# Kernel tuning notes

Hardware: AMD Instinct MI355X
Metric: run time of the kernel (lower is better)

The kernel has to match this reference:

```python
import jax, jax.numpy as jnp
import numpy as np

V, D, K, NH, FF, NV, MC, NL = 4096, 128, 3, 4, 512, 16384, 32, 2
HD = D // NH


def _ln(x, g, b):
    m = x.mean(-1, keepdims=True)
    v = ((x - m) ** 2).mean(-1, keepdims=True)
    return (x - m) / jnp.sqrt(v + 1e-5) * g + b


def setup_inputs() -> dict:
    key = jax.random.key(0)
    ks = iter(jax.random.split(key, 48))
    r = lambda shape, s=1.0: jax.random.normal(next(ks), shape, jnp.float32) * s
    inp = {}
    inp["visits"] = jax.random.randint(next(ks), (NV, MC), 0, V)
    inp["deltas"] = jax.random.uniform(next(ks), (NV,), jnp.float32) * 365.0
    inp["pad_idx"] = 0
    inp["X_hyp"] = r((V, D), 0.03)  # points inside unit Poincare ball
    inp["kernels"] = r((K, V, V), 1.0 / np.sqrt(V))
    inp["proj_W"] = r((K * D, D), 1.0 / np.sqrt(K * D))
    inp["proj_b"] = jnp.zeros((D,), jnp.float32)
    for nm in ["Wq", "Wk", "Wv", "Wo"]:
        inp[nm] = r((NL, D, D), 1.0 / np.sqrt(D))
    for nm in ["bq", "bk", "bv", "bo"]:
        inp[nm] = jnp.zeros((NL, D), jnp.float32)
    inp["ff_W1"] = r((NL, D, FF), 1.0 / np.sqrt(D))
    inp["ff_b1"] = jnp.zeros((NL, FF), jnp.float32)
    inp["ff_W2"] = r((NL, FF, D), 1.0 / np.sqrt(FF))
    inp["ff_b2"] = jnp.zeros((NL, D), jnp.float32)
    inp["ln1_g"] = jnp.ones((NL, D), jnp.float32)
    inp["ln1_b"] = jnp.zeros((NL, D), jnp.float32)
    inp["ln2_g"] = jnp.ones((NL, D), jnp.float32)
    inp["ln2_b"] = jnp.zeros((NL, D), jnp.float32)
    inp["tf_W"] = r((1, D))
    inp["tf_b"] = jnp.zeros((D,), jnp.float32)
    inp["tp_W"] = r((D, D), 1.0 / np.sqrt(D))
    inp["tp_b"] = jnp.zeros((D,), jnp.float32)
    return inp


def reference(visits, deltas, pad_idx, X_hyp, kernels, proj_W, proj_b,
              Wq, Wk, Wv, Wo, bq, bk, bv, bo,
              ff_W1, ff_b1, ff_W2, ff_b2,
              ln1_g, ln1_b, ln2_g, ln2_b,
              tf_W, tf_b, tp_W, tp_b):
    # --- hyperbolic logmap0 (Poincare ball, c=1) ---
    nrm = jnp.clip(jnp.linalg.norm(X_hyp, axis=-1, keepdims=True), 1e-7, 1.0 - 1e-5)
    Z0 = jnp.arctanh(nrm) * X_hyp / nrm  # [V, D]
    # --- multi-scale graph diffusion + projection ---
    Zk = jnp.einsum('kvu,ud->vkd', kernels, Z0).reshape(V, K * D)  # concat over scales
    H = Zk @ proj_W + proj_b  # [V, D]
    # --- global self-attention blocks over all codes (batch 1, L=V) ---
    x = H[None]  # [1, V, D]
    for i in range(NL):
        q = (x @ Wq[i] + bq[i]).reshape(1, V, NH, HD).transpose(0, 2, 1, 3)
        k = (x @ Wk[i] + bk[i]).reshape(1, V, NH, HD).transpose(0, 2, 1, 3)
        v = (x @ Wv[i] + bv[i]).reshape(1, V, NH, HD).transpose(0, 2, 1, 3)
        a = jax.nn.softmax(jnp.einsum('bhqd,bhkd->bhqk', q, k) / np.sqrt(HD), axis=-1)
        o = jnp.einsum('bhqk,bhkd->bhqd', a, v).transpose(0, 2, 1, 3).reshape(1, V, D)
        o = o @ Wo[i] + bo[i]
        x = _ln(x + o, ln1_g[i], ln1_b[i])
        f = jax.nn.gelu(x @ ff_W1[i] + ff_b1[i], approximate=False) @ ff_W2[i] + ff_b2[i]
        x = _ln(x + f, ln2_g[i], ln2_b[i])
    Hr = x[0]  # [V, D]
    # --- time embedding ---
    freq = (deltas[:, None] / 180.0) @ tf_W + tf_b  # [NV, D]
    te = (1.0 - jnp.tanh(freq) ** 2) @ tp_W + tp_b
    # --- ragged per-visit gather + masked mean (the fused-kernel target) ---
    mask = (visits != pad_idx)  # [NV, MC]
    hg = Hr[visits] * mask[..., None]  # [NV, MC, D]
    cnt = mask.sum(-1, keepdims=True)
    vis = hg.sum(1) / jnp.maximum(cnt, 1)  # empty visits -> zeros
    return vis + te
```

## Files before the change

kernel.cpp:

```cpp
#include <hip/hip_runtime.h>


using f16 = _Float16;
typedef f16   f16x8 __attribute__((ext_vector_type(8)));
typedef float f32x4 __attribute__((ext_vector_type(4)));

#define V_   4096
#define D_   128
#define NVIS 16384
#define KS_  8

union H4 { f16 h[4]; uint2 u; };

struct CvtTask { const float* src; void* dst; int R, C, kind; };
struct CvtTasks { CvtTask t[24]; int n; };

__global__ __launch_bounds__(256) void cvt_kernel(CvtTasks T) {
  int tid0 = blockIdx.x * 256 + threadIdx.x;
  int stride = gridDim.x * 256;
  for (int i = 0; i < T.n; i++) {
    CvtTask tk = T.t[i];
    int total = tk.R * tk.C;
    for (int idx = tid0; idx < total; idx += stride) {
      int r = idx / tk.C, c = idx - r * tk.C;
      if (tk.kind == 0)
        ((f16*)tk.dst)[(long long)c * tk.R + r] = (f16)tk.src[idx];
      else
        ((float*)tk.dst)[idx] = tk.src[idx];
    }
  }
}

__global__ __launch_bounds__(256) void logmap_kernel(const float* __restrict__ X, float* __restrict__ Z0) {
  int row = blockIdx.x * 4 + (threadIdx.x >> 6);
  int l = threadIdx.x & 63;
  const float* xr = X + (long long)row * D_;
  float a = xr[l], b = xr[l + 64];
  float ss = a * a + b * b;
  #pragma unroll
  for (int m = 1; m < 64; m <<= 1) ss += __shfl_xor(ss, m);
  float nrm = sqrtf(ss);
  float nc = fminf(fmaxf(nrm, 1e-7f), 1.0f - 1e-5f);
  float scale = atanhf(nc) / nc;
  float* zr = Z0 + (long long)row * D_;
  zr[l] = a * scale; zr[l + 64] = b * scale;
}

struct GemmP {
  const float* A;  long long a_y, a_z;  int lda;
  const f16*  BT;  long long bt_y, bt_z; int ldbt;
  const float* bias; int bias_y, bias_z;
  float* C;  long long c_y, c_z;   int ldc;
  f16*  CH;  long long ch_y, ch_z; int ldch;
  f16*  CHT; long long cht_y, cht_z; int ldcht;
  int K;
};

template<int ACT, bool WC, bool WH, bool WHT>
__global__ __launch_bounds__(256) void gemm_kernel(GemmP p) {
  __shared__ alignas(16) f16 As[64][64];
  __shared__ alignas(16) f16 Bs[128][64];
  int tid = threadIdx.x;
  int m0 = blockIdx.x * 64;
  long long by = blockIdx.y, bz = blockIdx.z;
  const float* A = p.A + by * p.a_y + bz * p.a_z + (long long)m0 * p.lda;
  const f16* BT  = p.BT + by * p.bt_y + bz * p.bt_z;

  int wid = tid >> 6, l = tid & 63;
  int lr = l & 15, lg = l >> 4;
  int wm = (wid & 1) * 32;
  int wn = (wid >> 1) * 64;

  f32x4 acc[2][4] = {};

  for (int kb = 0; kb < p.K; kb += 64) {
    __syncthreads();
    #pragma unroll
    for (int pi = 0; pi < 4; pi++) {
      int idx = pi * 256 + tid;
      int r = idx >> 4, c4 = (idx & 15) * 4;
      float4 v = *(const float4*)(A + (long long)r * p.lda + kb + c4);
      int cc = c4 ^ ((r & 7) << 3);
      H4 tmp; tmp.h[0] = (f16)v.x; tmp.h[1] = (f16)v.y; tmp.h[2] = (f16)v.z; tmp.h[3] = (f16)v.w;
      *(uint2*)&As[r][cc] = tmp.u;
    }
    #pragma unroll
    for (int pi = 0; pi < 4; pi++) {
      int idx = pi * 256 + tid;
      int n = idx >> 3, g8 = (idx & 7) * 8;
      f16x8 v = *(const f16x8*)(BT + (long long)n * p.ldbt + kb + g8);
      *(f16x8*)&Bs[n][g8 ^ ((n & 7) << 3)] = v;
    }
    __syncthreads();
    #pragma unroll
    for (int kk = 0; kk < 64; kk += 32) {
      f16x8 a[2], b[4];
      #pragma unroll
      for (int mt = 0; mt < 2; mt++) {
        int r = wm + mt * 16 + lr;
        a[mt] = *(const f16x8*)&As[r][(kk + lg * 8) ^ ((r & 7) << 3)];
      }
      #pragma unroll
      for (int nt = 0; nt < 4; nt++) {
        int n = wn + nt * 16 + lr;
        b[nt] = *(const f16x8*)&Bs[n][(kk + lg * 8) ^ ((n & 7) << 3)];
      }
      #pragma unroll
      for (int mt = 0; mt < 2; mt++)
        #pragma unroll
        for (int nt = 0; nt < 4; nt++)
          acc[mt][nt] = __builtin_amdgcn_mfma_f32_16x16x32_f16(a[mt], b[nt], acc[mt][nt], 0, 0, 0);
    }
  }

  const float* bias = p.bias ? p.bias + by * p.bias_y + bz * p.bias_z : nullptr;
  float* C = nullptr; f16* CH = nullptr; f16* CHT = nullptr;
  if (WC)  C   = p.C   + by * p.c_y   + bz * p.c_z   + (long long)m0 * p.ldc;
  if (WH)  CH  = p.CH  + by * p.ch_y  + bz * p.ch_z  + (long long)m0 * p.ldch;
  if (WHT) CHT = p.CHT + by * p.cht_y + bz * p.cht_z;

  #pragma unroll
  for (int nt = 0; nt < 4; nt++) {
    int n = wn + nt * 16 + lr;
    float bv = bias ? bias[n] : 0.0f;
    #pragma unroll
    for (int mt = 0; mt < 2; mt++) {
      H4 th;
      #pragma unroll
      for (int r = 0; r < 4; r++) {
        float val = acc[mt][nt][r] + bv;
        if (ACT == 1) val = 0.5f * val * (1.0f + erff(val * 0.70710678118654752f));
        int m = wm + mt * 16 + lg * 4 + r;
        if (WC) C[(long long)m * p.ldc + n] = val;
        if (WH) CH[(long long)m * p.ldch + n] = (f16)val;
        th.h[r] = (f16)val;
      }
      if (WHT)
        *(uint2*)&CHT[(long long)n * p.ldcht + m0 + wm + mt * 16 + lg * 4] = th.u;
    }
  }
}

__global__ __launch_bounds__(256) void combine_kernel(const float* __restrict__ Hp, const float* __restrict__ proj_b,
                                                      float* __restrict__ x) {
  int i = blockIdx.x * 256 + threadIdx.x;
  float s = proj_b[i & 127];
  #pragma unroll
  for (int j = 0; j < 12; j++) s += Hp[(long long)j * (V_ * D_) + i];
  x[i] = s;
}

__global__ __launch_bounds__(256) void attn_kernel(const f16* __restrict__ qh, const f16* __restrict__ kh,
                                                   const f16* __restrict__ vT,
                                                   float* __restrict__ Op, float* __restrict__ Ml) {
  __shared__ alignas(16) f16 Ks[64][40];
  __shared__ alignas(16) f16 Vs[32][72];
  __shared__ alignas(16) f16 Ps[4][16][72];
  int tid = threadIdx.x, w = tid >> 6, l = tid & 63, lr = l & 15, lg = l >> 4;
  int h = blockIdx.y, q0 = blockIdx.x * 64, z = blockIdx.z;
  const float sc = 0.17677669529663687f;

  f16x8 aq = *(const f16x8*)&qh[(long long)(q0 + w * 16 + lr) * D_ + h * 32 + lg * 8];
  float mrow[4], lsum[4];
  f32x4 oacc[2] = {};
  #pragma unroll
  for (int r = 0; r < 4; r++) { mrow[r] = -1e30f; lsum[r] = 0.f; }
  const f32x4 vzero = {0.f, 0.f, 0.f, 0.f};

  for (int kt = z * (V_ / 64 / KS_); kt < (z + 1) * (V_ / 64 / KS_); kt++) {
    int key0 = kt * 64;
    __syncthreads();
    {
      int key = tid >> 2, g8 = (tid & 3) * 8;
      *(f16x8*)&Ks[key][g8] = *(const f16x8*)&kh[(long long)(key0 + key) * D_ + h * 32 + g8];
      int dd = tid >> 3, kg = (tid & 7) * 8;
      *(f16x8*)&Vs[dd][kg] = *(const f16x8*)&vT[(long long)(h * 32 + dd) * V_ + key0 + kg];
    }
    __syncthreads();
    f32x4 s[4];
    #pragma unroll
    for (int t = 0; t < 4; t++) {
      f16x8 bk = *(const f16x8*)&Ks[t * 16 + lr][lg * 8];
      s[t] = __builtin_amdgcn_mfma_f32_16x16x32_f16(aq, bk, vzero, 0, 0, 0);
    }
    float pv[4][4];
    #pragma unroll
    for (int r = 0; r < 4; r++) {
      float sv0 = s[0][r] * sc, sv1 = s[1][r] * sc, sv2 = s[2][r] * sc, sv3 = s[3][r] * sc;
      float mx = fmaxf(fmaxf(sv0, sv1), fmaxf(sv2, sv3));
      #pragma unroll
      for (int msk = 1; msk < 16; msk <<= 1) mx = fmaxf(mx, __shfl_xor(mx, msk));
      float mn = fmaxf(mrow[r], mx);
      float alpha = expf(mrow[r] - mn);
      float e0 = expf(sv0 - mn), e1 = expf(sv1 - mn), e2 = expf(sv2 - mn), e3 = expf(sv3 - mn);
      pv[0][r] = e0; pv[1][r] = e1; pv[2][r] = e2; pv[3][r] = e3;
      float rs = e0 + e1 + e2 + e3;
      #pragma unroll
      for (int msk = 1; msk < 16; msk <<= 1) rs += __shfl_xor(rs, msk);
      lsum[r] = lsum[r] * alpha + rs;
      mrow[r] = mn;
      oacc[0][r] *= alpha; oacc[1][r] *= alpha;
    }
    #pragma unroll
    for (int t = 0; t < 4; t++)
      #pragma unroll
      for (int r = 0; r < 4; r++)
        Ps[w][lg * 4 + r][t * 16 + lr] = (f16)pv[t][r];
    #pragma unroll
    for (int kc = 0; kc < 2; kc++) {
      f16x8 pa = *(const f16x8*)&Ps[w][lr][kc * 32 + lg * 8];
      #pragma unroll
      for (int t = 0; t < 2; t++) {
        f16x8 bvv = *(const f16x8*)&Vs[t * 16 + lr][kc * 32 + lg * 8];
        oacc[t] = __builtin_amdgcn_mfma_f32_16x16x32_f16(pa, bvv, oacc[t], 0, 0, 0);
      }
    }
  }
  #pragma unroll
  for (int t = 0; t < 2; t++)
    #pragma unroll
    for (int r = 0; r < 4; r++) {
      int q = q0 + w * 16 + lg * 4 + r;
      Op[(long long)z * (V_ * D_) + (long long)q * D_ + h * 32 + t * 16 + lr] = oacc[t][r];
    }
  if (lr == 0) {
    #pragma unroll
    for (int r = 0; r < 4; r++) {
      int q = q0 + w * 16 + lg * 4 + r;
      Ml[(z * 4 + h) * V_ + q] = mrow[r];
      Ml[KS_ * 4 * V_ + (z * 4 + h) * V_ + q] = lsum[r];
    }
  }
}

__global__ __launch_bounds__(256) void attn_combine(const float* __restrict__ Op, const float* __restrict__ Ml,
                                                    float* __restrict__ o) {
  int i = blockIdx.x * 256 + threadIdx.x;
  int q = i >> 7, h = (i & 127) >> 5;
  float mv[KS_], lv[KS_];
  float m = -1e30f;
  #pragma unroll
  for (int s = 0; s < KS_; s++) {
    mv[s] = Ml[(s * 4 + h) * V_ + q];
    lv[s] = Ml[KS_ * 4 * V_ + (s * 4 + h) * V_ + q];
    m = fmaxf(m, mv[s]);
  }
  float L = 0.f, O = 0.f;
  #pragma unroll
  for (int s = 0; s < KS_; s++) {
    float wgt = expf(mv[s] - m);
    L += wgt * lv[s];
    O += wgt * Op[(long long)s * (V_ * D_) + i];
  }
  o[i] = O / L;
}

__global__ __launch_bounds__(256) void ln_kernel(float* __restrict__ x, const float* __restrict__ add,
                                                 const float* __restrict__ g, const float* __restrict__ b) {
  int row = blockIdx.x * 4 + (threadIdx.x >> 6);
  int l = threadIdx.x & 63;
  long long base = (long long)row * D_;
  float a = x[base + l] + add[base + l];
  float c = x[base + l + 64] + add[base + l + 64];
  float s = a + c, ss = a * a + c * c;
  #pragma unroll
  for (int m = 1; m < 64; m <<= 1) { s += __shfl_xor(s, m); ss += __shfl_xor(ss, m); }
  float mean = s * (1.0f / 128.0f);
  float var = ss * (1.0f / 128.0f) - mean * mean;
  float rstd = rsqrtf(var + 1e-5f);
  x[base + l]      = (a - mean) * rstd * g[l] + b[l];
  x[base + l + 64] = (c - mean) * rstd * g[l + 64] + b[l + 64];
}

__global__ __launch_bounds__(256) void timefeat_kernel(const float* __restrict__ deltas, const float* __restrict__ tf_W,
                                                       const float* __restrict__ tf_b, float* __restrict__ S) {
  int i = blockIdx.x * 256 + threadIdx.x;
  int n = i >> 7, d = i & 127;
  float fr = deltas[n] * (1.0f / 180.0f) * tf_W[d] + tf_b[d];
  float t = tanhf(fr);
  S[i] = 1.0f - t * t;
}

__global__ __launch_bounds__(256) void gather_kernel(const int* __restrict__ visits, const int* __restrict__ pad_ptr,
                                                     const float* __restrict__ Hr, float* __restrict__ out) {
  __shared__ int vis[2][32];
  int tid = threadIdx.x;
  int pad = *pad_ptr;
  int nb = blockIdx.x * 2;
  if (tid < 64) { int s = tid >> 5, c = tid & 31; vis[s][c] = visits[(long long)(nb + s) * 32 + c]; }
  __syncthreads();
  int s = tid >> 7, d = tid & 127;
  float acc = 0.f; int cnt = 0;
  #pragma unroll 8
  for (int c = 0; c < 32; c++) {
    int idx = vis[s][c];
    if (idx != pad) { acc += Hr[(long long)idx * D_ + d]; cnt++; }
  }
  long long oi = (long long)(nb + s) * D_ + d;
  out[oi] += acc / (float)(cnt > 0 ? cnt : 1);
}

extern "C" void kernel_launch(void* const* d_in, const int* in_sizes, int n_in,
                              void* d_out, int out_size, void* d_ws, size_t ws_size,
                              hipStream_t stream) {
  const int*   visits  = (const int*)d_in[0];
  const float* deltas  = (const float*)d_in[1];
  const int*   pad_idx = (const int*)d_in[2];
  const float* X_hyp   = (const float*)d_in[3];
  const float* kernels = (const float*)d_in[4];
  const float* proj_W  = (const float*)d_in[5];
  const float* proj_b  = (const float*)d_in[6];
  const float* Wq = (const float*)d_in[7];
  const float* Wk = (const float*)d_in[8];
  const float* Wv = (const float*)d_in[9];
  const float* Wo = (const float*)d_in[10];
  const float* bq = (const float*)d_in[11];
  const float* bk = (const float*)d_in[12];
  const float* bv = (const float*)d_in[13];
  const float* bo = (const float*)d_in[14];
  const float* ff_W1 = (const float*)d_in[15];
  const float* ff_b1 = (const float*)d_in[16];
  const float* ff_W2 = (const float*)d_in[17];
  const float* ff_b2 = (const float*)d_in[18];
  const float* ln1_g = (const float*)d_in[19];
  const float* ln1_b = (const float*)d_in[20];
  const float* ln2_g = (const float*)d_in[21];
  const float* ln2_b = (const float*)d_in[22];
  const float* tf_W  = (const float*)d_in[23];
  const float* tf_b  = (const float*)d_in[24];
  const float* tp_W  = (const float*)d_in[25];
  const float* tp_b  = (const float*)d_in[26];
  float* out = (float*)d_out;

  char* ws = (char*)d_ws;
  constexpr long long MB = 1ll << 20;
  f16*   projT = (f16*)(ws);
  f16*   qkvT  = (f16*)(ws + 98304);
  f16*   woT   = (f16*)(ws + 294912);
  f16*   w1T   = (f16*)(ws + 360448);
  f16*   w2T   = (f16*)(ws + 622592);
  f16*   tpT   = (f16*)(ws + 884736);
  float* bqkv  = (float*)(ws + 917504);
  float* Z0    = (float*)(ws + 1 * MB);
  f16*   ycatT = (f16*)(ws + 3 * MB);
  float* x     = (float*)(ws + 6 * MB);
  char*  big   = ws + 8 * MB;
  float* Hp    = (float*)big;
  f16*   qk_h  = (f16*)big;
  f16*   vT    = (f16*)(big + 2 * MB);
  float* o_    = (float*)(big + 3 * MB);
  float* oW    = (float*)(big + 5 * MB);
  float* Op    = (float*)(big + 7 * MB);
  float* Ml    = (float*)(big + 23 * MB);
  float* t_    = (float*)big;
  float* f_    = (float*)(big + 8 * MB);
  float* S_    = (float*)big;
  (void)ws_size; (void)in_sizes; (void)n_in; (void)out_size;

  CvtTasks T; int ntk = 0;
  auto addT = [&](const float* s, void* d, int R, int C, int kind) { T.t[ntk++] = {s, d, R, C, kind}; };
  for (int k = 0; k < 3; k++) addT(proj_W + k * 16384, projT + k * 16384, 128, 128, 0);
  for (int i = 0; i < 2; i++) {
    addT(Wq + i * 16384, qkvT + i * 49152 + 0,     128, 128, 0);
    addT(Wk + i * 16384, qkvT + i * 49152 + 16384, 128, 128, 0);
    addT(Wv + i * 16384, qkvT + i * 49152 + 32768, 128, 128, 0);
    addT(Wo + i * 16384, woT + i * 16384, 128, 128, 0);
    addT(ff_W1 + i * 65536, w1T + i * 65536, 128, 512, 0);
    addT(ff_W2 + i * 65536, w2T + i * 65536, 512, 128, 0);
    addT(bq + i * 128, bqkv + i * 384 + 0,   1, 128, 1);
    addT(bk + i * 128, bqkv + i * 384 + 128, 1, 128, 1);
    addT(bv + i * 128, bqkv + i * 384 + 256, 1, 128, 1);
  }
  addT(tp_W, tpT, 128, 128, 0);
  T.n = ntk;
  cvt_kernel<<<256, 256, 0, stream>>>(T);

  logmap_kernel<<<V_ / 4, 256, 0, stream>>>(X_hyp, Z0);

  {
    GemmP g{};
    g.A = Z0; g.lda = 128;
    g.BT = projT; g.ldbt = 128; g.bt_z = 16384;
    g.CHT = ycatT; g.ldcht = V_; g.cht_z = (long long)128 * V_;
    g.K = 128;
    gemm_kernel<0, false, false, true><<<dim3(64, 1, 3), 256, 0, stream>>>(g);
  }
  {
    GemmP g{};
    g.A = kernels; g.lda = V_; g.a_y = 1024; g.a_z = (long long)V_ * V_;
    g.BT = ycatT;  g.ldbt = V_; g.bt_y = 1024; g.bt_z = (long long)128 * V_;
    g.C = Hp; g.ldc = 128; g.c_y = (long long)V_ * D_; g.c_z = 4ll * V_ * D_;
    g.K = 1024;
    gemm_kernel<0, true, false, false><<<dim3(64, 4, 3), 256, 0, stream>>>(g);
  }
  combine_kernel<<<V_ * D_ / 256, 256, 0, stream>>>(Hp, proj_b, x);

  for (int i = 0; i < 2; i++) {
    {
      GemmP g{};
      g.A = x; g.lda = 128;
      g.BT = qkvT + i * 49152; g.ldbt = 128; g.bt_z = 16384;
      g.bias = bqkv + i * 384; g.bias_z = 128;
      g.CH = qk_h; g.ldch = 128; g.ch_z = (long long)V_ * D_;
      g.K = 128;
      gemm_kernel<0, false, true, false><<<dim3(64, 1, 2), 256, 0, stream>>>(g);
    }
    {
      GemmP g{};
      g.A = x; g.lda = 128;
      g.BT = qkvT + i * 49152 + 32768; g.ldbt = 128;
      g.bias = bqkv + i * 384 + 256;
      g.CHT = vT; g.ldcht = V_;
      g.K = 128;
      gemm_kernel<0, false, false, true><<<dim3(64, 1, 1), 256, 0, stream>>>(g);
    }
    attn_kernel<<<dim3(V_ / 64, 4, KS_), 256, 0, stream>>>(qk_h, qk_h + (long long)V_ * D_, vT, Op, Ml);
    attn_combine<<<V_ * D_ / 256, 256, 0, stream>>>(Op, Ml, o_);
    {
      GemmP g{};
      g.A = o_; g.lda = 128;
      g.BT = woT + i * 16384; g.ldbt = 128;
      g.bias = bo + i * 128;
      g.C = oW; g.ldc = 128;
      g.K = 128;
      gemm_kernel<0, true, false, false><<<dim3(64, 1, 1), 256, 0, stream>>>(g);
    }
    ln_kernel<<<V_ / 4, 256, 0, stream>>>(x, oW, ln1_g + i * 128, ln1_b + i * 128);
    {
      GemmP g{};
      g.A = x; g.lda = 128;
      g.BT = w1T + i * 65536; g.ldbt = 128; g.bt_y = 128 * 128;
      g.bias = ff_b1 + i * 512; g.bias_y = 128;
      g.C = t_; g.ldc = 512; g.c_y = 128;
      g.K = 128;
      gemm_kernel<1, true, false, false><<<dim3(64, 4, 1), 256, 0, stream>>>(g);
    }
    {
      GemmP g{};
      g.A = t_; g.lda = 512;
      g.BT = w2T + i * 65536; g.ldbt = 512;
      g.bias = ff_b2 + i * 128;
      g.C = f_; g.ldc = 128;
      g.K = 512;
      gemm_kernel<0, true, false, false><<<dim3(64, 1, 1), 256, 0, stream>>>(g);
    }
    ln_kernel<<<V_ / 4, 256, 0, stream>>>(x, f_, ln2_g + i * 128, ln2_b + i * 128);
  }

  timefeat_kernel<<<NVIS * D_ / 256, 256, 0, stream>>>(deltas, tf_W, tf_b, S_);
  {
    GemmP g{};
    g.A = S_; g.lda = 128;
    g.BT = tpT; g.ldbt = 128;
    g.bias = tp_b;
    g.C = out; g.ldc = 128;
    g.K = 128;
    gemm_kernel<0, true, false, false><<<dim3(NVIS / 64, 1, 1), 256, 0, stream>>>(g);
  }
  gather_kernel<<<NVIS / 2, 256, 0, stream>>>(visits, pad_idx, x, out);
}
```

Baseline: 708.9 us.

## Fuse residual+LayerNorm into GEMM epilogue, merge QKV GEMMs, transpose attention softmax

Moves the residual add and LayerNorm into the Wo and FF2 GEMM epilogues, reducing row statistics across warps through shared memory, and removes the separate ln_kernel launches and intermediate buffers. Merges the QK and V projection GEMMs into one launch with per-z output modes. Computes attention scores transposed so each lane owns one query row, cutting the per-row shuffle reductions and allowing vectorized P stores. This adds a __syncthreads and extra shared memory to the GEMM epilogue.

Result: faster. 640.0 us (-9.7%).

```diff
diff --git a/kernel.cpp b/kernel.cpp
--- a/kernel.cpp
+++ b/kernel.cpp
@@ -53,13 +53,15 @@
   float* C;  long long c_y, c_z;   int ldc;
   f16*  CH;  long long ch_y, ch_z; int ldch;
   f16*  CHT; long long cht_y, cht_z; int ldcht;
+  const float* lng; const float* lnb;
   int K;
 };
 
-template<int ACT, bool WC, bool WH, bool WHT>
+template<int EPI>
 __global__ __launch_bounds__(256) void gemm_kernel(GemmP p) {
   __shared__ alignas(16) f16 As[64][64];
   __shared__ alignas(16) f16 Bs[128][64];
+  __shared__ float lnred[2][64][2];
   int tid = threadIdx.x;
   int m0 = blockIdx.x * 64;
   long long by = blockIdx.y, bz = blockIdx.z;
@@ -114,29 +116,80 @@
   }
 
   const float* bias = p.bias ? p.bias + by * p.bias_y + bz * p.bias_z : nullptr;
-  float* C = nullptr; f16* CH = nullptr; f16* CHT = nullptr;
-  if (WC)  C   = p.C   + by * p.c_y   + bz * p.c_z   + (long long)m0 * p.ldc;
-  if (WH)  CH  = p.CH  + by * p.ch_y  + bz * p.ch_z  + (long long)m0 * p.ldch;
-  if (WHT) CHT = p.CHT + by * p.cht_y + bz * p.cht_z;
-
-  #pragma unroll
-  for (int nt = 0; nt < 4; nt++) {
-    int n = wn + nt * 16 + lr;
-    float bv = bias ? bias[n] : 0.0f;
-    #pragma unroll
-    for (int mt = 0; mt < 2; mt++) {
-      H4 th;
+
+  if constexpr (EPI == 5) {
+    float* C = p.C + (long long)m0 * p.ldc;
+    #pragma unroll
+    for (int nt = 0; nt < 4; nt++) {
+      int n = wn + nt * 16 + lr;
+      float bv = bias ? bias[n] : 0.0f;
+      #pragma unroll
+      for (int mt = 0; mt < 2; mt++)
+        #pragma unroll
+        for (int r = 0; r < 4; r++) {
+          int m = wm + mt * 16 + lg * 4 + r;
+          acc[mt][nt][r] += bv + C[(long long)m * p.ldc + n];
+        }
+    }
+    #pragma unroll
+    for (int mt = 0; mt < 2; mt++)
       #pragma unroll
       for (int r = 0; r < 4; r++) {
-        float val = acc[mt][nt][r] + bv;
-        if (ACT == 1) val = 0.5f * val * (1.0f + erff(val * 0.70710678118654752f));
-        int m = wm + mt * 16 + lg * 4 + r;
-        if (WC) C[(long long)m * p.ldc + n] = val;
-        if (WH) CH[(long long)m * p.ldch + n] = (f16)val;
-        th.h[r] = (f16)val;
-      }
-      if (WHT)
-        *(uint2*)&CHT[(long long)n * p.ldcht + m0 + wm + mt * 16 + lg * 4] = th.u;
+        float s = 0.f, ss = 0.f;
+        #pragma unroll
+        for (int nt = 0; nt < 4; nt++) { float v = acc[mt][nt][r]; s += v; ss += v * v; }
+        #pragma unroll
+        for (int msk = 1; msk < 16; msk <<= 1) { s += __shfl_xor(s, msk); ss += __shfl_xor(ss, msk); }
+        if (lr == 0) {
+          int row = wm + mt * 16 + lg * 4 + r;
+          lnred[wid >> 1][row][0] = s; lnred[wid >> 1][row][1] = ss;
+        }
+      }
+    __syncthreads();
+    #pragma unroll
+    for (int mt = 0; mt < 2; mt++)
+      #pragma unroll
+      for (int r = 0; r < 4; r++) {
+        int row = wm + mt * 16 + lg * 4 + r;
+        float s  = lnred[0][row][0] + lnred[1][row][0];
+        float ss = lnred[0][row][1] + lnred[1][row][1];
+        float mean = s * (1.0f / 128.0f);
+        float rstd = rsqrtf(ss * (1.0f / 128.0f) - mean * mean + 1e-5f);
+        #pragma unroll
+        for (int nt = 0; nt < 4; nt++) {
+          int n = wn + nt * 16 + lr;
+          C[(long long)row * p.ldc + n] = (acc[mt][nt][r] - mean) * rstd * p.lng[n] + p.lnb[n];
+        }
+      }
+    return;
+  } else {
+    bool do_c  = (EPI == 0 || EPI == 1);
+    bool do_h  = (EPI == 4 && bz < 2);
+    bool do_ht = (EPI == 3) || (EPI == 4 && bz == 2);
+    float* C = nullptr; f16* CH = nullptr; f16* CHT = nullptr;
+    if (do_c)  C   = p.C   + by * p.c_y   + bz * p.c_z   + (long long)m0 * p.ldc;
+    if (do_h)  CH  = p.CH  + by * p.ch_y  + bz * p.ch_z  + (long long)m0 * p.ldch;
+    if (do_ht) CHT = p.CHT + by * p.cht_y + bz * p.cht_z;
+
+    #pragma unroll
+    for (int nt = 0; nt < 4; nt++) {
+      int n = wn + nt * 16 + lr;
+      float bv = bias ? bias[n] : 0.0f;
+      #pragma unroll
+      for (int mt = 0; mt < 2; mt++) {
+        H4 th;
+        #pragma unroll
+        for (int r = 0; r < 4; r++) {
+          float val = acc[mt][nt][r] + bv;
+          if (EPI == 1) val = 0.5f * val * (1.0f + erff(val * 0.70710678118654752f));
+          int m = wm + mt * 16 + lg * 4 + r;
+          if (do_c) C[(long long)m * p.ldc + n] = val;
+          if (do_h) CH[(long long)m * p.ldch + n] = (f16)val;
+          th.h[r] = (f16)val;
+        }
+        if (do_ht)
+          *(uint2*)&CHT[(long long)n * p.ldcht + m0 + wm + mt * 16 + lg * 4] = th.u;
+      }
     }
   }
 }
@@ -161,10 +214,8 @@
   const float sc = 0.17677669529663687f;
 
   f16x8 aq = *(const f16x8*)&qh[(long long)(q0 + w * 16 + lr) * D_ + h * 32 + lg * 8];
-  float mrow[4], lsum[4];
+  float mrow = -1e30f, lsum = 0.f;
   f32x4 oacc[2] = {};
-  #pragma unroll
-  for (int r = 0; r < 4; r++) { mrow[r] = -1e30f; lsum[r] = 0.f; }
   const f32x4 vzero = {0.f, 0.f, 0.f, 0.f};
 
   for (int kt = z * (V_ / 64 / KS_); kt < (z + 1) * (V_ / 64 / KS_); kt++) {
@@ -177,35 +228,43 @@
       *(f16x8*)&Vs[dd][kg] = *(const f16x8*)&vT[(long long)(h * 32 + dd) * V_ + key0 + kg];
     }
     __syncthreads();
-    f32x4 s[4];
+    f32x4 st[4];
     #pragma unroll
     for (int t = 0; t < 4; t++) {
       f16x8 bk = *(const f16x8*)&Ks[t * 16 + lr][lg * 8];
-      s[t] = __builtin_amdgcn_mfma_f32_16x16x32_f16(aq, bk, vzero, 0, 0, 0);
-    }
-    float pv[4][4];
+      st[t] = __builtin_amdgcn_mfma_f32_16x16x32_f16(bk, aq, vzero, 0, 0, 0);
+    }
+    float sv[16];
+    #pragma unroll
+    for (int t = 0; t < 4; t++)
+      #pragma unroll
+      for (int r = 0; r < 4; r++) sv[t * 4 + r] = st[t][r] * sc;
+    float mx = sv[0];
+    #pragma unroll
+    for (int i = 1; i < 16; i++) mx = fmaxf(mx, sv[i]);
+    mx = fmaxf(mx, __shfl_xor(mx, 16));
+    mx = fmaxf(mx, __shfl_xor(mx, 32));
+    float mn = fmaxf(mrow, mx);
+    float alpha = expf(mrow - mn);
+    mrow = mn;
+    float rs = 0.f, pv[16];
+    #pragma unroll
+    for (int i = 0; i < 16; i++) { pv[i] = expf(sv[i] - mn); rs += pv[i]; }
+    rs += __shfl_xor(rs, 16);
+    rs += __shfl_xor(rs, 32);
+    lsum = lsum * alpha + rs;
     #pragma unroll
     for (int r = 0; r < 4; r++) {
-      float sv0 = s[0][r] * sc, sv1 = s[1][r] * sc, sv2 = s[2][r] * sc, sv3 = s[3][r] * sc;
-      float mx = fmaxf(fmaxf(sv0, sv1), fmaxf(sv2, sv3));
-      #pragma unroll
-      for (int msk = 1; msk < 16; msk <<= 1) mx = fmaxf(mx, __shfl_xor(mx, msk));
-      float mn = fmaxf(mrow[r], mx);
-      float alpha = expf(mrow[r] - mn);
-      float e0 = expf(sv0 - mn), e1 = expf(sv1 - mn), e2 = expf(sv2 - mn), e3 = expf(sv3 - mn);
-      pv[0][r] = e0; pv[1][r] = e1; pv[2][r] = e2; pv[3][r] = e3;
-      float rs = e0 + e1 + e2 + e3;
-      #pragma unroll
-      for (int msk = 1; msk < 16; msk <<= 1) rs += __shfl_xor(rs, msk);
-      lsum[r] = lsum[r] * alpha + rs;
-      mrow[r] = mn;
-      oacc[0][r] *= alpha; oacc[1][r] *= alpha;
-    }
-    #pragma unroll
-    for (int t = 0; t < 4; t++)
-      #pragma unroll
-      for (int r = 0; r < 4; r++)
-        Ps[w][lg * 4 + r][t * 16 + lr] = (f16)pv[t][r];
+      float ar = __shfl(alpha, lg * 4 + r);
+      oacc[0][r] *= ar; oacc[1][r] *= ar;
+    }
+    #pragma unroll
+    for (int t = 0; t < 4; t++) {
+      H4 hh;
+      #pragma unroll
+      for (int r = 0; r < 4; r++) hh.h[r] = (f16)pv[t * 4 + r];
+      *(uint2*)&Ps[w][lr][t * 16 + lg * 4] = hh.u;
+    }
     #pragma unroll
     for (int kc = 0; kc < 2; kc++) {
       f16x8 pa = *(const f16x8*)&Ps[w][lr][kc * 32 + lg * 8];
@@ -223,13 +282,10 @@
       int q = q0 + w * 16 + lg * 4 + r;
       Op[(long long)z * (V_ * D_) + (long long)q * D_ + h * 32 + t * 16 + lr] = oacc[t][r];
     }
-  if (lr == 0) {
-    #pragma unroll
-    for (int r = 0; r < 4; r++) {
-      int q = q0 + w * 16 + lg * 4 + r;
-      Ml[(z * 4 + h) * V_ + q] = mrow[r];
-      Ml[KS_ * 4 * V_ + (z * 4 + h) * V_ + q] = lsum[r];
-    }
+  if (l < 16) {
+    int q = q0 + w * 16 + l;
+    Ml[(z * 4 + h) * V_ + q] = mrow;
+    Ml[KS_ * 4 * V_ + (z * 4 + h) * V_ + q] = lsum;
   }
 }
 
@@ -253,23 +309,6 @@
     O += wgt * Op[(long long)s * (V_ * D_) + i];
   }
   o[i] = O / L;
-}
-
-__global__ __launch_bounds__(256) void ln_kernel(float* __restrict__ x, const float* __restrict__ add,
-                                                 const float* __restrict__ g, const float* __restrict__ b) {
-  int row = blockIdx.x * 4 + (threadIdx.x >> 6);
-  int l = threadIdx.x & 63;
-  long long base = (long long)row * D_;
-  float a = x[base + l] + add[base + l];
-  float c = x[base + l + 64] + add[base + l + 64];
-  float s = a + c, ss = a * a + c * c;
-  #pragma unroll
-  for (int m = 1; m < 64; m <<= 1) { s += __shfl_xor(s, m); ss += __shfl_xor(ss, m); }
-  float mean = s * (1.0f / 128.0f);
-  float var = ss * (1.0f / 128.0f) - mean * mean;
-  float rstd = rsqrtf(var + 1e-5f);
-  x[base + l]      = (a - mean) * rstd * g[l] + b[l];
-  x[base + l + 64] = (c - mean) * rstd * g[l + 64] + b[l + 64];
 }
 
 __global__ __launch_bounds__(256) void timefeat_kernel(const float* __restrict__ deltas, const float* __restrict__ tf_W,
@@ -349,11 +388,9 @@
   f16*   qk_h  = (f16*)big;
   f16*   vT    = (f16*)(big + 2 * MB);
   float* o_    = (float*)(big + 3 * MB);
-  float* oW    = (float*)(big + 5 * MB);
   float* Op    = (float*)(big + 7 * MB);
   float* Ml    = (float*)(big + 23 * MB);
   float* t_    = (float*)big;
-  float* f_    = (float*)(big + 8 * MB);
   float* S_    = (float*)big;
   (void)ws_size; (void)in_sizes; (void)n_in; (void)out_size;
 
@@ -383,7 +420,7 @@
     g.BT = projT; g.ldbt = 128; g.bt_z = 16384;
     g.CHT = ycatT; g.ldcht = V_; g.cht_z = (long long)128 * V_;
     g.K = 128;
-    gemm_kernel<0, false, false, true><<<dim3(64, 1, 3), 256, 0, stream>>>(g);
+    gemm_kernel<3><<<dim3(64, 1, 3), 256, 0, stream>>>(g);
   }
   {
     GemmP g{};
@@ -391,7 +428,7 @@
     g.BT = ycatT;  g.ldbt = V_; g.bt_y = 1024; g.bt_z = (long long)128 * V_;
     g.C = Hp; g.ldc = 128; g.c_y = (long long)V_ * D_; g.c_z = 4ll * V_ * D_;
     g.K = 1024;
-    gemm_kernel<0, true, false, false><<<dim3(64, 4, 3), 256, 0, stream>>>(g);
+    gemm_kernel<0><<<dim3(64, 4, 3), 256, 0, stream>>>(g);
   }
   combine_kernel<<<V_ * D_ / 256, 256, 0, stream>>>(Hp, proj_b, x);
 
@@ -402,17 +439,9 @@
       g.BT = qkvT + i * 49152; g.ldbt = 128; g.bt_z = 16384;
       g.bias = bqkv + i * 384; g.bias_z = 128;
       g.CH = qk_h; g.ldch = 128; g.ch_z = (long long)V_ * D_;
+      g.CHT = vT; g.ldcht = V_; g.cht_z = 0;
       g.K = 128;
-      gemm_kernel<0, false, true, false><<<dim3(64, 1, 2), 256, 0, stream>>>(g);
-    }
-    {
-      GemmP g{};
-      g.A = x; g.lda = 128;
-      g.BT = qkvT + i * 49152 + 32768; g.ldbt = 128;
-      g.bias = bqkv + i * 384 + 256;
-      g.CHT = vT; g.ldcht = V_;
-      g.K = 128;
-      gemm_kernel<0, false, false, true><<<dim3(64, 1, 1), 256, 0, stream>>>(g);
+      gemm_kernel<4><<<dim3(64, 1, 3), 256, 0, stream>>>(g);
     }
     attn_kernel<<<dim3(V_ / 64, 4, KS_), 256, 0, stream>>>(qk_h, qk_h + (long long)V_ * D_, vT, Op, Ml);
     attn_combine<<<V_ * D_ / 256, 256, 0, stream>>>(Op, Ml, o_);
@@ -421,11 +450,11 @@
       g.A = o_; g.lda = 128;
       g.BT = woT + i * 16384; g.ldbt = 128;
       g.bias = bo + i * 128;
-      g.C = oW; g.ldc = 128;
+      g.C = x; g.ldc = 128;
+      g.lng = ln1_g + i * 128; g.lnb = ln1_b + i * 128;
       g.K = 128;
-      gemm_kernel<0, true, false, false><<<dim3(64, 1, 1), 256, 0, stream>>>(g);
-    }
-    ln_kernel<<<V_ / 4, 256, 0, stream>>>(x, oW, ln1_g + i * 128, ln1_b + i * 128);
+      gemm_kernel<5><<<dim3(64, 1, 1), 256, 0, stream>>>(g);
+    }
     {
       GemmP g{};
       g.A = x; g.lda = 128;
@@ -433,18 +462,18 @@
       g.bias = ff_b1 + i * 512; g.bias_y = 128;
       g.C = t_; g.ldc = 512; g.c_y = 128;
       g.K = 128;
-      gemm_kernel<1, true, false, false><<<dim3(64, 4, 1), 256, 0, stream>>>(g);
+      gemm_kernel<1><<<dim3(64, 4, 1), 256, 0, stream>>>(g);
     }
     {
       GemmP g{};
       g.A = t_; g.lda = 512;
       g.BT = w2T + i * 65536; g.ldbt = 512;
       g.bias = ff_b2 + i * 128;
-      g.C = f_; g.ldc = 128;
+      g.C = x; g.ldc = 128;
+      g.lng = ln2_g + i * 128; g.lnb = ln2_b + i * 128;
       g.K = 512;
-      gemm_kernel<0, true, false, false><<<dim3(64, 1, 1), 256, 0, stream>>>(g);
-    }
-    ln_kernel<<<V_ / 4, 256, 0, stream>>>(x, f_, ln2_g + i * 128, ln2_b + i * 128);
+      gemm_kernel<5><<<dim3(64, 1, 1), 256, 0, stream>>>(g);
+    }
   }
 
   timefeat_kernel<<<NVIS * D_ / 256, 256, 0, stream>>>(deltas, tf_W, tf_b, S_);
@@ -455,7 +484,7 @@
     g.bias = tp_b;
     g.C = out; g.ldc = 128;
     g.K = 128;
-    gemm_kernel<0, true, false, false><<<dim3(NVIS / 64, 1, 1), 256, 0, stream>>>(g);
+    gemm_kernel<0><<<dim3(NVIS / 64, 1, 1), 256, 0, stream>>>(g);
   }
   gather_kernel<<<NVIS / 2, 256, 0, stream>>>(visits, pad_idx, x, out);
 }
```
